# Kernel optimization log

Hardware: AMD Instinct MI355X
Metric: run time of the kernel (lower is better)

The kernel has to match this reference:

```python
import jax, jax.numpy as jnp
import numpy as np

M_BITS = 4            # mem_pot_bits
M_MASK = (1 << M_BITS) - 1
T_MASK = (1 << 4) - 1  # t_bits = 4
ALPHA = 0.5


def setup_inputs() -> dict:
    key = jax.random.key(0)
    ks = jax.random.split(key, 8)
    B, N_IN, N_OUT, M = 256, 4096, 4096, 1 << M_BITS
    return {
        "active_mask": jax.random.randint(ks[0], (B, N_IN), 0, 2, dtype=jnp.int32),
        "t": 7,
        "prev_neuron_id": jax.random.randint(ks[1], (N_IN,), 0, M, dtype=jnp.int32),
        "t_last": jnp.zeros((B,), jnp.int32),
        "mem_fict": jax.random.uniform(ks[2], (B, N_OUT), jnp.float32),
        "mem_phys": jax.random.randint(ks[3], (B, N_OUT), 0, M, dtype=jnp.int32),
        "accumulate_lut_delta": jnp.zeros((N_OUT, M), jnp.float32),
        "tau": jax.random.uniform(ks[4], (N_OUT,), jnp.float32),
        "v_th": jax.random.uniform(ks[5], (N_OUT,), jnp.float32),
        "syn_w": jax.random.uniform(ks[6], (N_IN, N_OUT), jnp.float32),
        "mem_map": jax.nn.sigmoid(jax.random.normal(ks[7], (N_OUT, M), jnp.float32)),
    }


def reference(active_mask, t, prev_neuron_id, t_last, mem_fict, mem_phys,
              accumulate_lut_delta, tau, v_th, syn_w, mem_map):
    # delta_t = (t - t_last) & t_bit_mask  (Python '&' binds looser than '-')
    delta_t = (t - t_last) & T_MASK                          # (B,)
    t_last_new = jnp.full_like(t_last, t)

    # masked matmul + exponential membrane decay
    weights_sum = active_mask.astype(jnp.float32) @ syn_w    # (B, N_out)
    decay = jnp.exp(-tau[None, :] * delta_t[:, None].astype(jnp.float32))
    mem_fict_new = mem_fict * decay + weights_sum

    # XOR tree-reduction over masked input ids == bitwise parity per bit.
    # Only the low M_BITS matter (result is masked by m_bit_mask afterwards).
    masked_ids = jnp.where(active_mask.astype(bool), prev_neuron_id[None, :], 0)
    shifts = jnp.arange(M_BITS, dtype=jnp.int32)
    bits = (masked_ids[:, :, None] >> shifts) & 1            # (B, N_in, M_BITS)
    parity = jnp.sum(bits, axis=1) & 1                       # (B, M_BITS)
    acc = jnp.sum(parity << shifts, axis=1)                  # (B,)

    # physical membrane update (all low-bit integer ops)
    mem_phys_new = (mem_phys ^ delta_t[:, None] ^ acc[:, None]) & M_MASK

    # LUT gather + threshold
    n_out = mem_map.shape[0]
    rows = jnp.broadcast_to(jnp.arange(n_out)[None, :], mem_phys_new.shape)
    v_map_vals = mem_map[rows, mem_phys_new]                 # (B, N_out)
    active_next = v_map_vals >= v_th[None, :]

    # scatter-add per-bucket LUT delta (alpha != 0 path)
    delta = ALPHA * (mem_phys_new.astype(jnp.float32) - v_map_vals)
    lut_new = accumulate_lut_delta.at[rows, mem_phys_new].add(delta)

    return active_next, mem_fict_new, mem_phys_new, lut_new, t_last_new
```

## Files before the change

kernel.cpp:

```cpp
#include <hip/hip_runtime.h>

typedef __attribute__((ext_vector_type(8))) short short8;
typedef __attribute__((ext_vector_type(4))) float f32x4;
typedef unsigned int u32;

#define N_IN  4096
#define N_OUT 4096
#define NBAT  256

#define OUT_ACT   0
#define OUT_FICT  1048576
#define OUT_PHYS  2097152
#define OUT_LUT   3145728
#define OUT_TLAST 3211264

#define WS_AIMG   0
#define WS_PART   2097152
#define WS_DTF    (WS_PART + 16777216)
#define WS_DXA    (WS_DTF + 1024)

#define BM 128
#define BN 32
#define BK 64
#define SPLITK 4
#define KCHUNK (N_IN / SPLITK)
#define NTK (KCHUNK / BK)

__device__ __forceinline__ unsigned f2bf(float f) {
  unsigned u = __float_as_uint(f);
  return (u + 0x7FFFu + ((u >> 16) & 1u)) >> 16;
}

__global__ __launch_bounds__(256) void snn_pre(
    const int* __restrict__ mask, const int* __restrict__ t_ptr,
    const int* __restrict__ pid, const int* __restrict__ t_last,
    float* __restrict__ dtf_ws, int* __restrict__ dxa_ws,
    char* __restrict__ aimg, float* __restrict__ out)
{
  const int b = blockIdx.x, tid = threadIdx.x;
  const int k0 = tid * 16;
  const int4* mp = (const int4*)(mask + (size_t)b * N_IN + k0);
  const int4* pp = (const int4*)(pid + k0);
  int x = 0;
  u32 wv[8];
#pragma unroll
  for (int q = 0; q < 4; ++q) {
    int4 m = mp[q];
    int4 id = pp[q];
    x ^= (m.x ? id.x : 0) ^ (m.y ? id.y : 0) ^ (m.z ? id.z : 0) ^ (m.w ? id.w : 0);
    wv[q * 2]     = (m.x ? 0x3F80u : 0u) | ((m.y ? 0x3F80u : 0u) << 16);
    wv[q * 2 + 1] = (m.z ? 0x3F80u : 0u) | ((m.w ? 0x3F80u : 0u) << 16);
  }
  {
    const int rg = b >> 5, rl = b & 31;
    const int mi = rl >> 4, l15 = rl & 15;
    const int ktg = tid >> 2, kk = (tid >> 1) & 1, l4_0 = (tid & 1) * 2;
    char* base = aimg + ((size_t)((rg * 64 + ktg) * 4 + kk * 2 + mi) << 10);
    uint4 v0; v0.x = wv[0]; v0.y = wv[1]; v0.z = wv[2]; v0.w = wv[3];
    uint4 v1; v1.x = wv[4]; v1.y = wv[5]; v1.z = wv[6]; v1.w = wv[7];
    *(uint4*)(base + (l4_0 * 16 + l15) * 16)       = v0;
    *(uint4*)(base + ((l4_0 + 1) * 16 + l15) * 16) = v1;
  }
  x ^= __shfl_xor(x, 32); x ^= __shfl_xor(x, 16); x ^= __shfl_xor(x, 8);
  x ^= __shfl_xor(x, 4);  x ^= __shfl_xor(x, 2);  x ^= __shfl_xor(x, 1);
  __shared__ int wx[4];
  if ((tid & 63) == 0) wx[tid >> 6] = x;
  __syncthreads();
  if (tid == 0) {
    int acc = wx[0] ^ wx[1] ^ wx[2] ^ wx[3];
    int tt = t_ptr[0];
    int dt = (tt - t_last[b]) & 15;
    dtf_ws[b] = (float)dt;
    dxa_ws[b] = dt ^ (acc & 15);
    out[OUT_TLAST + b] = (float)tt;
  }
}

__global__ __launch_bounds__(256) void snn_gemm(
    const char* __restrict__ aimg, const float* __restrict__ synw,
    float* __restrict__ part)
{
  __shared__ __align__(16) char ldsB[2][BN * BK * 2];

  const int tid = threadIdx.x;
  const int lane = tid & 63, wid = tid >> 6;
  const int l15 = lane & 15, l4 = lane >> 4;

  const int bid = blockIdx.x;
  const int sid = (bid & 7) * 128 + (bid >> 3);
  const int nb = sid >> 3;
  const int mb = (sid >> 2) & 1;
  const int kc = sid & 3;
  const int bmb = mb * BM, bnb = nb * BN, kcb = kc * KCHUNK;
  const int rg = mb * 4 + wid;

  const char* a_base = aimg + (((size_t)(rg * 64 + kc * 16) * 4) << 10) + lane * 16;

  const int b_rr = (tid & 31) * 2;
  const int b_n0 = (tid >> 5) * 4;
  const float* b_base = synw + ((size_t)(kcb + b_rr) << 12) + bnb + b_n0;

  auto loadA = [&](int t, uint4* d) {
    const char* p = a_base + ((size_t)t << 12);
#pragma unroll
    for (int f = 0; f < 4; ++f) d[f] = *(const uint4*)(p + (f << 10));
  };
  auto loadB = [&](int t, float4* d) {
    const float* p = b_base + ((size_t)t << 18);
    d[0] = *(const float4*)(p);
    d[1] = *(const float4*)(p + 4096);
  };
  auto writeB = [&](const float4* v, int buf) {
    const float* r0 = (const float*)&v[0];
    const float* r1 = (const float*)&v[1];
#pragma unroll
    for (int i = 0; i < 4; ++i) {
      int n = b_n0 + i;
      u32 pk = f2bf(r0[i]) | (f2bf(r1[i]) << 16);
      *(u32*)(&ldsB[buf][n * 128 + (((b_rr >> 3) ^ (n & 7)) << 4) + ((b_rr & 7) << 1)]) = pk;
    }
  };

  f32x4 acc[2][2] = {};

  auto compute = [&](int buf, const uint4* af) {
#pragma unroll
    for (int kk = 0; kk < 2; ++kk) {
      const int g0 = kk * 4 + l4;
      short8 a[2], b[2];
#pragma unroll
      for (int mi = 0; mi < 2; ++mi)
        a[mi] = *(const short8*)&af[kk * 2 + mi];
#pragma unroll
      for (int nj = 0; nj < 2; ++nj) {
        int col = nj * 16 + l15;
        b[nj] = *(const short8*)(&ldsB[buf][col * 128 + ((g0 ^ (col & 7)) << 4)]);
      }
#pragma unroll
      for (int mi = 0; mi < 2; ++mi)
#pragma unroll
        for (int nj = 0; nj < 2; ++nj)
          acc[mi][nj] = __builtin_amdgcn_mfma_f32_16x16x32_bf16(a[mi], b[nj], acc[mi][nj], 0, 0, 0);
    }
  };

  uint4  aA[4], aB[4];
  float4 bA[2], bB[2];

  loadB(0, bA); loadA(0, aA);
  loadB(1, bB); loadA(1, aB);

#define PHASE(T, BV, AV, BUF)                                 \
  {                                                           \
    writeB(BV, BUF);                                          \
    if ((T) + 2 < NTK) loadB((T) + 2, BV);                    \
    asm volatile("s_waitcnt lgkmcnt(0)" ::: "memory");        \
    __builtin_amdgcn_s_barrier();                             \
    __builtin_amdgcn_sched_barrier(0);                        \
    compute(BUF, AV);                                         \
    if ((T) + 2 < NTK) loadA((T) + 2, AV);                    \
  }

  for (int t = 0; t < NTK; t += 2) {
    PHASE(t,     bA, aA, 0)
    PHASE(t + 1, bB, aB, 1)
  }
#undef PHASE

  float* pb = part + (size_t)kc * (NBAT * N_OUT);
#pragma unroll
  for (int mi = 0; mi < 2; ++mi)
#pragma unroll
    for (int nj = 0; nj < 2; ++nj) {
      const int o = bnb + nj * 16 + l15;
#pragma unroll
      for (int r = 0; r < 4; ++r) {
        const int b = bmb + wid * 32 + mi * 16 + l4 * 4 + r;
        pb[(size_t)b * N_OUT + o] = acc[mi][nj][r];
      }
    }
}

__global__ __launch_bounds__(256) void snn_reduce(
    const float* __restrict__ part, const float* __restrict__ memf,
    const int* __restrict__ memp, const float* __restrict__ tau,
    const float* __restrict__ vth, const float* __restrict__ mem_map,
    const float* __restrict__ dtf_ws, const int* __restrict__ dxa_ws,
    float* __restrict__ out)
{
  const int flat = (blockIdx.x * 256 + threadIdx.x) * 4;
  const int b = flat >> 12, o = flat & 4095;
  const float4 p0 = *(const float4*)(part + flat);
  const float4 p1 = *(const float4*)(part + 1048576 + flat);
  const float4 p2 = *(const float4*)(part + 2097152 + flat);
  const float4 p3 = *(const float4*)(part + 3145728 + flat);
  float4 ws;
  ws.x = (p0.x + p1.x) + (p2.x + p3.x);
  ws.y = (p0.y + p1.y) + (p2.y + p3.y);
  ws.z = (p0.z + p1.z) + (p2.z + p3.z);
  ws.w = (p0.w + p1.w) + (p2.w + p3.w);
  const float dtf = dtf_ws[b];
  const int dxa = dxa_ws[b];
  const float4 mf = *(const float4*)(memf + flat);
  const int4  mp = *(const int4*)(memp + flat);
  const float4 tv = *(const float4*)(tau + o);
  const float4 vv = *(const float4*)(vth + o);
  float4 act, fict, phys;
#define DO(c, oi) { float d = __expf(-tv.c * dtf); fict.c = mf.c * d + ws.c; \
                    int mpn = (mp.c ^ dxa) & 15; phys.c = (float)mpn; \
                    act.c = (mem_map[(o + oi) * 16 + mpn] >= vv.c) ? 1.f : 0.f; }
  DO(x, 0) DO(y, 1) DO(z, 2) DO(w, 3)
#undef DO
  *(float4*)(out + OUT_ACT  + flat) = act;
  *(float4*)(out + OUT_FICT + flat) = fict;
  *(float4*)(out + OUT_PHYS + flat) = phys;
}

__global__ __launch_bounds__(256) void snn_lut(
    const int* __restrict__ memp, const int* __restrict__ dxa_ws,
    const float* __restrict__ mem_map, const float* __restrict__ lut_in,
    float* __restrict__ out)
{
  __shared__ int mp[NBAT * 16];
  __shared__ int dxs[NBAT];
  const int tid = threadIdx.x;
  const int o0 = blockIdx.x * 16;
#pragma unroll
  for (int i = 0; i < 16; ++i) {
    int b = i * 16 + (tid >> 4);
    int oj = tid & 15;
    mp[b * 16 + oj] = memp[(size_t)b * N_OUT + o0 + oj];
  }
  dxs[tid] = dxa_ws[tid];
  __syncthreads();
  const int o_l = tid >> 4, m = tid & 15;
  int cnt = 0;
#pragma unroll 8
  for (int b = 0; b < NBAT; ++b) {
    int v = (mp[b * 16 + o_l] ^ dxs[b]) & 15;
    cnt += (v == m);
  }
  const int o = o0 + o_l;
  const float vmap = mem_map[o * 16 + m];
  out[OUT_LUT + o * 16 + m] = lut_in[o * 16 + m] + 0.5f * ((float)m - vmap) * (float)cnt;
}

extern "C" void kernel_launch(void* const* d_in, const int* in_sizes, int n_in,
                              void* d_out, int out_size, void* d_ws, size_t ws_size,
                              hipStream_t stream)
{
  const int*   mask    = (const int*)d_in[0];
  const int*   t_ptr   = (const int*)d_in[1];
  const int*   pid     = (const int*)d_in[2];
  const int*   t_last  = (const int*)d_in[3];
  const float* memf    = (const float*)d_in[4];
  const int*   memp    = (const int*)d_in[5];
  const float* lut_in  = (const float*)d_in[6];
  const float* tau     = (const float*)d_in[7];
  const float* vth     = (const float*)d_in[8];
  const float* synw    = (const float*)d_in[9];
  const float* mem_map = (const float*)d_in[10];
  float* out = (float*)d_out;

  char* wsb = (char*)d_ws;
  char*  aimg   = wsb + WS_AIMG;
  float* part   = (float*)(wsb + WS_PART);
  float* dtf_ws = (float*)(wsb + WS_DTF);
  int*   dxa_ws = (int*)(wsb + WS_DXA);

  snn_pre<<<NBAT, 256, 0, stream>>>(mask, t_ptr, pid, t_last, dtf_ws, dxa_ws, aimg, out);
  snn_gemm<<<(NBAT / BM) * (N_OUT / BN) * SPLITK, 256, 0, stream>>>(
      aimg, synw, part);
  snn_reduce<<<(NBAT * N_OUT) / 1024, 256, 0, stream>>>(
      part, memf, memp, tau, vth, mem_map, dtf_ws, dxa_ws, out);
  snn_lut<<<NBAT, 256, 0, stream>>>(memp, dxa_ws, mem_map, lut_in, out);
}
```

Before: 55.19 us.

## Pre-convert syn_w into a bf16 MFMA fragment image and drop LDS staging in GEMM

```diff
diff --git a/kernel.cpp b/kernel.cpp
--- a/kernel.cpp
+++ b/kernel.cpp
@@ -15,7 +15,8 @@
 #define OUT_TLAST 3211264
 
 #define WS_AIMG   0
-#define WS_PART   2097152
+#define WS_BIMG   2097152
+#define WS_PART   (WS_BIMG + 33554432)
 #define WS_DTF    (WS_PART + 16777216)
 #define WS_DXA    (WS_DTF + 1024)
 
@@ -76,12 +77,51 @@
   }
 }
 
+__global__ __launch_bounds__(256) void snn_conv(
+    const float* __restrict__ synw, char* __restrict__ bimg)
+{
+  __shared__ float ldsf[64 * 132];
+  const int tid = threadIdx.x;
+  const int kt = blockIdx.x & 63, nbg = blockIdx.x >> 6;
+
+  const float* src = synw + ((size_t)kt * 64) * N_OUT + nbg * 128;
+  {
+    const int r0 = tid >> 5, ch = tid & 31;
+#pragma unroll
+    for (int i = 0; i < 8; ++i) {
+      int row = i * 8 + r0;
+      float4 v = *(const float4*)(src + (size_t)row * N_OUT + ch * 4);
+      *(float4*)(&ldsf[row * 132 + ch * 4]) = v;
+    }
+  }
+  __syncthreads();
+
+  const int q = tid >> 6;
+  const int lane = tid & 63;
+  const int l15 = lane & 15, l4 = lane >> 4;
+  const int nb = nbg * 4 + q;
+  char* dst = bimg + (((size_t)(nb * 64 + kt) * 4) << 10) + lane * 16;
+
+#pragma unroll
+  for (int kk = 0; kk < 2; ++kk)
+#pragma unroll
+    for (int nj = 0; nj < 2; ++nj) {
+      const int col = q * 32 + nj * 16 + l15;
+      const int kb = kk * 32 + l4 * 8;
+      u32 w[4];
+#pragma unroll
+      for (int p = 0; p < 4; ++p)
+        w[p] = f2bf(ldsf[(kb + 2 * p) * 132 + col]) |
+               (f2bf(ldsf[(kb + 2 * p + 1) * 132 + col]) << 16);
+      uint4 v; v.x = w[0]; v.y = w[1]; v.z = w[2]; v.w = w[3];
+      *(uint4*)(dst + ((kk * 2 + nj) << 10)) = v;
+    }
+}
+
 __global__ __launch_bounds__(256) void snn_gemm(
-    const char* __restrict__ aimg, const float* __restrict__ synw,
+    const char* __restrict__ aimg, const char* __restrict__ bimg,
     float* __restrict__ part)
 {
-  __shared__ __align__(16) char ldsB[2][BN * BK * 2];
-
   const int tid = threadIdx.x;
   const int lane = tid & 63, wid = tid >> 6;
   const int l15 = lane & 15, l4 = lane >> 4;
@@ -91,81 +131,47 @@
   const int nb = sid >> 3;
   const int mb = (sid >> 2) & 1;
   const int kc = sid & 3;
-  const int bmb = mb * BM, bnb = nb * BN, kcb = kc * KCHUNK;
+  const int bmb = mb * BM, bnb = nb * BN;
   const int rg = mb * 4 + wid;
 
   const char* a_base = aimg + (((size_t)(rg * 64 + kc * 16) * 4) << 10) + lane * 16;
-
-  const int b_rr = (tid & 31) * 2;
-  const int b_n0 = (tid >> 5) * 4;
-  const float* b_base = synw + ((size_t)(kcb + b_rr) << 12) + bnb + b_n0;
+  const char* b_base = bimg + (((size_t)(nb * 64 + kc * 16) * 4) << 10) + lane * 16;
 
   auto loadA = [&](int t, uint4* d) {
     const char* p = a_base + ((size_t)t << 12);
 #pragma unroll
     for (int f = 0; f < 4; ++f) d[f] = *(const uint4*)(p + (f << 10));
   };
-  auto loadB = [&](int t, float4* d) {
-    const float* p = b_base + ((size_t)t << 18);
-    d[0] = *(const float4*)(p);
-    d[1] = *(const float4*)(p + 4096);
+  auto loadB = [&](int t, uint4* d) {
+    const char* p = b_base + ((size_t)t << 12);
+#pragma unroll
+    for (int f = 0; f < 4; ++f) d[f] = *(const uint4*)(p + (f << 10));
   };
-  auto writeB = [&](const float4* v, int buf) {
-    const float* r0 = (const float*)&v[0];
-    const float* r1 = (const float*)&v[1];
-#pragma unroll
-    for (int i = 0; i < 4; ++i) {
-      int n = b_n0 + i;
-      u32 pk = f2bf(r0[i]) | (f2bf(r1[i]) << 16);
-      *(u32*)(&ldsB[buf][n * 128 + (((b_rr >> 3) ^ (n & 7)) << 4) + ((b_rr & 7) << 1)]) = pk;
-    }
+
+  f32x4 acc[2][2] = {};
+
+  auto compute = [&](const uint4* af, const uint4* bf) {
+#pragma unroll
+    for (int kk = 0; kk < 2; ++kk)
+#pragma unroll
+      for (int mi = 0; mi < 2; ++mi)
+#pragma unroll
+        for (int nj = 0; nj < 2; ++nj)
+          acc[mi][nj] = __builtin_amdgcn_mfma_f32_16x16x32_bf16(
+              *(const short8*)&af[kk * 2 + mi],
+              *(const short8*)&bf[kk * 2 + nj], acc[mi][nj], 0, 0, 0);
   };
 
-  f32x4 acc[2][2] = {};
-
-  auto compute = [&](int buf, const uint4* af) {
-#pragma unroll
-    for (int kk = 0; kk < 2; ++kk) {
-      const int g0 = kk * 4 + l4;
-      short8 a[2], b[2];
-#pragma unroll
-      for (int mi = 0; mi < 2; ++mi)
-        a[mi] = *(const short8*)&af[kk * 2 + mi];
-#pragma unroll
-      for (int nj = 0; nj < 2; ++nj) {
-        int col = nj * 16 + l15;
-        b[nj] = *(const short8*)(&ldsB[buf][col * 128 + ((g0 ^ (col & 7)) << 4)]);
-      }
-#pragma unroll
-      for (int mi = 0; mi < 2; ++mi)
-#pragma unroll
-        for (int nj = 0; nj < 2; ++nj)
-          acc[mi][nj] = __builtin_amdgcn_mfma_f32_16x16x32_bf16(a[mi], b[nj], acc[mi][nj], 0, 0, 0);
-    }
-  };
-
-  uint4  aA[4], aB[4];
-  float4 bA[2], bB[2];
-
-  loadB(0, bA); loadA(0, aA);
-  loadB(1, bB); loadA(1, aB);
-
-#define PHASE(T, BV, AV, BUF)                                 \
-  {                                                           \
-    writeB(BV, BUF);                                          \
-    if ((T) + 2 < NTK) loadB((T) + 2, BV);                    \
-    asm volatile("s_waitcnt lgkmcnt(0)" ::: "memory");        \
-    __builtin_amdgcn_s_barrier();                             \
-    __builtin_amdgcn_sched_barrier(0);                        \
-    compute(BUF, AV);                                         \
-    if ((T) + 2 < NTK) loadA((T) + 2, AV);                    \
-  }
+  uint4 aP[4], bP[4], aQ[4], bQ[4];
+  loadA(0, aP); loadB(0, bP);
+  loadA(1, aQ); loadB(1, bQ);
 
   for (int t = 0; t < NTK; t += 2) {
-    PHASE(t,     bA, aA, 0)
-    PHASE(t + 1, bB, aB, 1)
-  }
-#undef PHASE
+    compute(aP, bP);
+    if (t + 2 < NTK) { loadA(t + 2, aP); loadB(t + 2, bP); }
+    compute(aQ, bQ);
+    if (t + 3 < NTK) { loadA(t + 3, aQ); loadB(t + 3, bQ); }
+  }
 
   float* pb = part + (size_t)kc * (NBAT * N_OUT);
 #pragma unroll
@@ -264,13 +270,15 @@
 
   char* wsb = (char*)d_ws;
   char*  aimg   = wsb + WS_AIMG;
+  char*  bimg   = wsb + WS_BIMG;
   float* part   = (float*)(wsb + WS_PART);
   float* dtf_ws = (float*)(wsb + WS_DTF);
   int*   dxa_ws = (int*)(wsb + WS_DXA);
 
   snn_pre<<<NBAT, 256, 0, stream>>>(mask, t_ptr, pid, t_last, dtf_ws, dxa_ws, aimg, out);
+  snn_conv<<<64 * 32, 256, 0, stream>>>(synw, bimg);
   snn_gemm<<<(NBAT / BM) * (N_OUT / BN) * SPLITK, 256, 0, stream>>>(
-      aimg, synw, part);
+      aimg, bimg, part);
   snn_reduce<<<(NBAT * N_OUT) / 1024, 256, 0, stream>>>(
       part, memf, memp, tau, vth, mem_map, dtf_ws, dxa_ws, out);
   snn_lut<<<NBAT, 256, 0, stream>>>(memp, dxa_ws, mem_map, lut_in, out);
```

New measurement: 62.67 us. 1.14x slower.
